# Optimization experiments

Hardware: AMD Instinct MI355X
Metric: run time of the kernel (lower is better)

The kernel has to match this reference:

```python
import jax, jax.numpy as jnp
import numpy as np

N_NODES = 50000
N_EDGES = 800000
IN_DIM = 64
OUT_DIM = 64
EDGE_DIM = 16
LN_EPS = 1e-5


def setup_inputs() -> dict:
    key = jax.random.key(0)
    ks = jax.random.split(key, 12)
    def lin(k, fan_in, fan_out):
        # torch nn.Linear default init: U(-1/sqrt(fan_in), 1/sqrt(fan_in))
        kw, kb = jax.random.split(k)
        bound = 1.0 / np.sqrt(fan_in)
        W = jax.random.uniform(kw, (fan_in, fan_out), jnp.float32, -bound, bound)
        b = jax.random.uniform(kb, (fan_out,), jnp.float32, -bound, bound)
        return W, b
    x = jax.random.normal(ks[0], (N_NODES, IN_DIM), jnp.float32)
    edge_index = jax.random.randint(ks[1], (2, N_EDGES), 0, N_NODES, jnp.int64 if jax.config.jax_enable_x64 else jnp.int32)
    edge_features = jax.random.normal(ks[2], (N_EDGES, EDGE_DIM), jnp.float32)
    W1, b1 = lin(ks[3], IN_DIM + EDGE_DIM, OUT_DIM)   # msg_mlp layer 1
    W2, b2 = lin(ks[4], OUT_DIM, OUT_DIM)             # msg_mlp layer 2
    W3, b3 = lin(ks[5], IN_DIM + OUT_DIM, OUT_DIM)    # update_mlp
    gamma = jnp.ones((OUT_DIM,), jnp.float32)
    beta = jnp.zeros((OUT_DIM,), jnp.float32)
    return {"x": x, "edge_index": edge_index, "edge_features": edge_features,
            "W1": W1, "b1": b1, "W2": W2, "b2": b2, "W3": W3, "b3": b3,
            "gamma": gamma, "beta": beta}


def reference(x, edge_index, edge_features, W1, b1, W2, b2, W3, b3, gamma, beta):
    num_nodes = x.shape[0]
    src, dst = edge_index[0], edge_index[1]
    # gather source node feats, concat with edge feats -> message MLP
    msg_in = jnp.concatenate([x[src], edge_features], axis=-1)           # [E, in+edge]
    h = jax.nn.relu(msg_in @ W1 + b1)
    messages = h @ W2 + b2                                               # [E, out]
    # scatter-add aggregate + mean by in-degree (count + 1e-8)
    agg = jax.ops.segment_sum(messages, dst, num_segments=num_nodes)     # [N, out]
    cnt = jax.ops.segment_sum(jnp.ones((messages.shape[0],), x.dtype), dst,
                              num_segments=num_nodes)[:, None]           # [N, 1]
    agg = agg / (cnt + 1e-8)
    # update MLP + residual (Identity since in_dim == out_dim) + LayerNorm
    updated = jax.nn.relu(jnp.concatenate([x, agg], axis=-1) @ W3 + b3)  # [N, out]
    y = updated + x
    mu = jnp.mean(y, axis=-1, keepdims=True)
    var = jnp.var(y, axis=-1, keepdims=True)
    return (y - mu) * jax.lax.rsqrt(var + LN_EPS) * gamma + beta
```

## Files before the change

kernel.cpp:

```cpp
#include <hip/hip_runtime.h>

typedef unsigned short u16;
typedef unsigned int u32;
typedef short short8 __attribute__((ext_vector_type(8)));
typedef short short4v __attribute__((ext_vector_type(4)));
typedef float floatx4 __attribute__((ext_vector_type(4)));

#define NE 800000
#define NNODES 50000
#define NBLK 196

#define LDS_FENCE() __asm__ volatile("s_waitcnt lgkmcnt(0)" ::: "memory")

__device__ __forceinline__ u16 f2bf(float f) {
    union { float f; unsigned int i; } v; v.f = f;
    return (u16)((v.i + 0x7fffu + ((v.i >> 16) & 1u)) >> 16);
}
__device__ __forceinline__ float bf2f(u16 u) {
    union { unsigned int i; float f; } v; v.i = ((unsigned int)u) << 16; return v.f;
}
__device__ __forceinline__ short8 pack8(const float4 a, const float4 b) {
    short8 o;
    o[0] = (short)f2bf(a.x); o[1] = (short)f2bf(a.y);
    o[2] = (short)f2bf(a.z); o[3] = (short)f2bf(a.w);
    o[4] = (short)f2bf(b.x); o[5] = (short)f2bf(b.y);
    o[6] = (short)f2bf(b.z); o[7] = (short)f2bf(b.w);
    return o;
}
__device__ __forceinline__ short8 ld8_bf(const float* __restrict__ p) {
    return pack8(*(const float4*)p, *(const float4*)(p + 4));
}

#define MFMA16(a, b, c) __builtin_amdgcn_mfma_f32_16x16x32_bf16(a, b, c, 0, 0, 0)

__global__ __launch_bounds__(256) void prep_kernel(
    const float* __restrict__ x, const int* __restrict__ ei,
    int* __restrict__ hist, u16* __restrict__ xbf)
{
    const int id = blockIdx.x * 256 + threadIdx.x;
    if (id < NE) atomicAdd(&hist[ei[NE + id]], 1);
    if (id < NNODES * 8) {
        *(short8*)&xbf[(size_t)id * 8] = ld8_bf(x + (size_t)id * 8);
    }
}

__global__ __launch_bounds__(256) void scan1_kernel(
    const int* __restrict__ hist, int* __restrict__ cursor, int* __restrict__ bsum)
{
    const int i = blockIdx.x * 256 + threadIdx.x;
    const int lane = threadIdx.x & 63;
    const int w = threadIdx.x >> 6;
    const int v = (i < NNODES) ? hist[i] : 0;
    int inc = v;
    #pragma unroll
    for (int o = 1; o < 64; o <<= 1) {
        const int tt = __shfl_up(inc, o);
        if (lane >= o) inc += tt;
    }
    __shared__ int ws[4];
    if (lane == 63) ws[w] = inc;
    __syncthreads();
    int add = 0;
    for (int j = 0; j < w; ++j) add += ws[j];
    const int excl = inc - v + add;
    if (i < NNODES) cursor[i] = excl;
    if (threadIdx.x == 255) bsum[blockIdx.x] = excl + v;
}

__global__ __launch_bounds__(256) void scan2_kernel(
    const int* __restrict__ bsum, int* __restrict__ bsumx)
{
    const int tid = threadIdx.x;
    const int lane = tid & 63;
    const int w = tid >> 6;
    const int v = (tid < NBLK) ? bsum[tid] : 0;
    int inc = v;
    #pragma unroll
    for (int o = 1; o < 64; o <<= 1) {
        const int tt = __shfl_up(inc, o);
        if (lane >= o) inc += tt;
    }
    __shared__ int ws[4];
    if (lane == 63) ws[w] = inc;
    __syncthreads();
    int add = 0;
    for (int j = 0; j < w; ++j) add += ws[j];
    bsumx[tid] = inc - v + add;
}

__global__ __launch_bounds__(256) void scatter_kernel(
    const int* __restrict__ ei, int* __restrict__ cursor,
    const int* __restrict__ bsumx, uint2* __restrict__ sde)
{
    const int e = blockIdx.x * 256 + threadIdx.x;
    if (e < NE) {
        const int dst = ei[NE + e];
        const int p = atomicAdd(&cursor[dst], 1) + bsumx[dst >> 8];
        uint2 v;
        v.x = (u32)e;
        v.y = ((u32)ei[e] << 16) | (u32)dst;
        sde[p] = v;
    }
}

__global__ __launch_bounds__(256) void edge_kernel(
    const u16* __restrict__ xbf, const float* __restrict__ ef,
    const float* __restrict__ w1, const float* __restrict__ b1,
    const float* __restrict__ w2, const float* __restrict__ b2,
    const uint2* __restrict__ sde, float* __restrict__ agg)
{
    constexpr int S1 = 104;
    constexpr int S2 = 72;
    __shared__ u16 A1[4][16 * S1];
    __shared__ u16 Hs[4][16 * S2];
    __shared__ int Ds[4][16];
    __shared__ u16 W2f[2][4][64 * 8];

    const int wid  = threadIdx.x >> 6;
    const int lane = threadIdx.x & 63;
    const int q    = lane >> 4;
    const int c    = lane & 15;
    const int r4   = lane >> 2;
    const int p4   = lane & 3;

    short8 w1f[3][4];
    #pragma unroll
    for (int kk = 0; kk < 3; ++kk)
        #pragma unroll
        for (int nn = 0; nn < 4; ++nn)
            #pragma unroll
            for (int j = 0; j < 8; ++j) {
                const int k = kk * 32 + q * 8 + j;
                w1f[kk][nn][j] = (k < 80) ? (short)f2bf(w1[k * 64 + nn * 16 + c]) : (short)0;
            }
    if (wid == 0) {
        #pragma unroll
        for (int kk = 0; kk < 2; ++kk)
            #pragma unroll
            for (int nn = 0; nn < 4; ++nn) {
                short8 f;
                #pragma unroll
                for (int j = 0; j < 8; ++j) {
                    const int k = kk * 32 + q * 8 + j;
                    f[j] = (short)f2bf(w2[k * 64 + nn * 16 + c]);
                }
                *(short8*)&W2f[kk][nn][lane * 8] = f;
            }
    }
    float b1v[4], b2v[4];
    #pragma unroll
    for (int nn = 0; nn < 4; ++nn) {
        b1v[nn] = b1[nn * 16 + c];
        b2v[nn] = b2[nn * 16 + c];
    }
    if (q == 1) {
        const short8 z8 = {0, 0, 0, 0, 0, 0, 0, 0};
        *(short8*)&A1[wid][c * S1 + 80] = z8;
        *(short8*)&A1[wid][c * S1 + 88] = z8;
    }
    __syncthreads();

    const floatx4 zero = {0.f, 0.f, 0.f, 0.f};
    const int ntile = NE / 16;
    const int stride = gridDim.x * 4;
    int t = blockIdx.x * 4 + wid;

    uint2 sdB; u32 eB;
    short8 xa, xb; float4 ev;
    int dcur;
    {
        const uint2 sdA = sde[t * 16 + c];
        const u32  eA  = sde[t * 16 + r4].x;
        dcur = (int)(sdA.y & 0xffffu);
        const int sA = (int)(sdA.y >> 16);
        int tb = t + stride; if (tb >= ntile) tb = ntile - 1;
        sdB = sde[tb * 16 + c];
        eB  = sde[tb * 16 + r4].x;
        const u16* xp = xbf + (size_t)sA * 64 + q * 16;
        xa = *(const short8*)xp;
        xb = *(const short8*)(xp + 8);
        ev = *(const float4*)(ef + (size_t)eA * 16 + p4 * 4);
    }

    for (; t < ntile; t += stride) {
        u16* arow = &A1[wid][c * S1 + q * 16];
        *(short8*)arow       = xa;
        *(short8*)(arow + 8) = xb;
        {
            short4v e4;
            e4[0] = (short)f2bf(ev.x); e4[1] = (short)f2bf(ev.y);
            e4[2] = (short)f2bf(ev.z); e4[3] = (short)f2bf(ev.w);
            *(short4v*)&A1[wid][r4 * S1 + 64 + p4 * 4] = e4;
        }
        if (q == 0) Ds[wid][c] = dcur;
        LDS_FENCE();

        short8 a1k[3];
        #pragma unroll
        for (int kk = 0; kk < 3; ++kk)
            a1k[kk] = *(const short8*)&A1[wid][c * S1 + kk * 32 + q * 8];

        const int dnext = (int)(sdB.y & 0xffffu);
        {
            const int sN = (int)(sdB.y >> 16);
            const u16* xp = xbf + (size_t)sN * 64 + q * 16;
            xa = *(const short8*)xp;
            xb = *(const short8*)(xp + 8);
            ev = *(const float4*)(ef + (size_t)eB * 16 + p4 * 4);
        }
        {
            int tb = t + 2 * stride; if (tb >= ntile) tb = ntile - 1;
            sdB = sde[tb * 16 + c];
            eB  = sde[tb * 16 + r4].x;
        }

        #pragma unroll
        for (int nn = 0; nn < 4; ++nn) {
            floatx4 acc = MFMA16(a1k[0], w1f[0][nn], zero);
            acc = MFMA16(a1k[1], w1f[1][nn], acc);
            acc = MFMA16(a1k[2], w1f[2][nn], acc);
            #pragma unroll
            for (int r = 0; r < 4; ++r) {
                const float h = fmaxf(acc[r] + b1v[nn], 0.f);
                Hs[wid][(q * 4 + r) * S2 + nn * 16 + c] = f2bf(h);
            }
        }
        LDS_FENCE();

        short8 a2k[2];
        #pragma unroll
        for (int kk = 0; kk < 2; ++kk)
            a2k[kk] = *(const short8*)&Hs[wid][c * S2 + kk * 32 + q * 8];

        #pragma unroll
        for (int nn = 0; nn < 4; ++nn) {
            const short8 wf0 = *(const short8*)&W2f[0][nn][lane * 8];
            const short8 wf1 = *(const short8*)&W2f[1][nn][lane * 8];
            floatx4 mg = MFMA16(a2k[0], wf0, zero);
            mg = MFMA16(a2k[1], wf1, mg);
            #pragma unroll
            for (int r = 0; r < 4; ++r)
                Hs[wid][(q * 4 + r) * S2 + nn * 16 + c] = f2bf(mg[r] + b2v[nn]);
        }
        LDS_FENCE();

        int dc = Ds[wid][0];
        float acc = bf2f(Hs[wid][lane]);
        #pragma unroll
        for (int row = 1; row < 16; ++row) {
            const int d = Ds[wid][row];
            const float v = bf2f(Hs[wid][row * S2 + lane]);
            if (d == dc) {
                acc += v;
            } else {
                atomicAdd(&agg[(size_t)dc * 64 + lane], acc);
                dc = d;
                acc = v;
            }
        }
        atomicAdd(&agg[(size_t)dc * 64 + lane], acc);

        dcur = dnext;
    }
}

__global__ __launch_bounds__(256) void node_kernel(
    const u16* __restrict__ xbf, const float* __restrict__ w3,
    const float* __restrict__ b3, const float* __restrict__ g,
    const float* __restrict__ bb, const float* __restrict__ agg,
    const int* __restrict__ hist, float* __restrict__ out)
{
    constexpr int S3 = 136;
    __shared__ u16 Cs[4][16 * S3];

    const int wid  = threadIdx.x >> 6;
    const int lane = threadIdx.x & 63;
    const int q    = lane >> 4;
    const int c    = lane & 15;

    short8 w3f[4][4];
    #pragma unroll
    for (int kk = 0; kk < 4; ++kk)
        #pragma unroll
        for (int nn = 0; nn < 4; ++nn)
            #pragma unroll
            for (int j = 0; j < 8; ++j) {
                const int k = kk * 32 + q * 8 + j;
                w3f[kk][nn][j] = (short)f2bf(w3[k * 64 + nn * 16 + c]);
            }
    float b3v[4], gv[4], bv[4];
    #pragma unroll
    for (int nn = 0; nn < 4; ++nn) {
        b3v[nn] = b3[nn * 16 + c];
        gv[nn]  = g[nn * 16 + c];
        bv[nn]  = bb[nn * 16 + c];
    }

    const floatx4 zero = {0.f, 0.f, 0.f, 0.f};
    const int ntile = NNODES / 16;

    for (int t = blockIdx.x * 4 + wid; t < ntile; t += gridDim.x * 4) {
        const int n0 = t * 16;
        const int node = n0 + c;
        u16* crow = &Cs[wid][c * S3];

        if (q < 2) {
            const u16* xp = xbf + (size_t)node * 64 + q * 32;
            *(short8*)&crow[q * 32]      = *(const short8*)xp;
            *(short8*)&crow[q * 32 + 8]  = *(const short8*)(xp + 8);
            *(short8*)&crow[q * 32 + 16] = *(const short8*)(xp + 16);
            *(short8*)&crow[q * 32 + 24] = *(const short8*)(xp + 24);
        } else {
            const int p = q - 2;
            const float inv = 1.0f / ((float)hist[node] + 1e-8f);
            const float* ap = agg + (size_t)node * 64 + p * 32;
            #pragma unroll
            for (int gi = 0; gi < 4; ++gi) {
                const float4 v0 = *(const float4*)(ap + gi * 8);
                const float4 v1 = *(const float4*)(ap + gi * 8 + 4);
                short8 o;
                o[0] = (short)f2bf(v0.x * inv);
                o[1] = (short)f2bf(v0.y * inv);
                o[2] = (short)f2bf(v0.z * inv);
                o[3] = (short)f2bf(v0.w * inv);
                o[4] = (short)f2bf(v1.x * inv);
                o[5] = (short)f2bf(v1.y * inv);
                o[6] = (short)f2bf(v1.z * inv);
                o[7] = (short)f2bf(v1.w * inv);
                *(short8*)&crow[64 + p * 32 + gi * 8] = o;
            }
        }
        LDS_FENCE();

        short8 af[4];
        #pragma unroll
        for (int kk = 0; kk < 4; ++kk)
            af[kk] = *(const short8*)&Cs[wid][c * S3 + kk * 32 + q * 8];

        float y[4][4];
        float s[4]  = {0.f, 0.f, 0.f, 0.f};
        float ss[4] = {0.f, 0.f, 0.f, 0.f};
        #pragma unroll
        for (int nn = 0; nn < 4; ++nn) {
            floatx4 acc = MFMA16(af[0], w3f[0][nn], zero);
            acc = MFMA16(af[1], w3f[1][nn], acc);
            acc = MFMA16(af[2], w3f[2][nn], acc);
            acc = MFMA16(af[3], w3f[3][nn], acc);
            #pragma unroll
            for (int r = 0; r < 4; ++r) {
                const float upd = fmaxf(acc[r] + b3v[nn], 0.f);
                const float xv = bf2f(Cs[wid][(q * 4 + r) * S3 + nn * 16 + c]);
                const float yy = upd + xv;
                y[r][nn] = yy;
                s[r] += yy;
                ss[r] += yy * yy;
            }
        }

        #pragma unroll
        for (int r = 0; r < 4; ++r) {
            float sr = s[r], sq = ss[r];
            #pragma unroll
            for (int off = 1; off < 16; off <<= 1) {
                sr += __shfl_xor(sr, off);
                sq += __shfl_xor(sq, off);
            }
            const float mu  = sr * (1.0f / 64.0f);
            const float var = sq * (1.0f / 64.0f) - mu * mu;
            const float rs  = rsqrtf(var + 1e-5f);
            float* op = out + (size_t)(n0 + q * 4 + r) * 64 + c;
            #pragma unroll
            for (int nn = 0; nn < 4; ++nn)
                op[nn * 16] = (y[r][nn] - mu) * rs * gv[nn] + bv[nn];
        }
    }
}

extern "C" void kernel_launch(void* const* d_in, const int* in_sizes, int n_in,
                              void* d_out, int out_size, void* d_ws, size_t ws_size,
                              hipStream_t stream) {
    const float* x   = (const float*)d_in[0];
    const int*   ei  = (const int*)d_in[1];
    const float* ef  = (const float*)d_in[2];
    const float* w1  = (const float*)d_in[3];
    const float* b1  = (const float*)d_in[4];
    const float* w2  = (const float*)d_in[5];
    const float* b2  = (const float*)d_in[6];
    const float* w3  = (const float*)d_in[7];
    const float* b3  = (const float*)d_in[8];
    const float* g   = (const float*)d_in[9];
    const float* bb  = (const float*)d_in[10];

    float* agg   = (float*)d_ws;
    int* hist    = (int*)d_ws + 3200000;
    int* cursor  = hist + NNODES;
    int* bsum    = cursor + NNODES;
    int* bsumx   = bsum + 256;
    u16* xbf     = (u16*)(bsumx + 256);
    uint2* sde   = (uint2*)((int*)d_ws + 4900512);

    hipMemsetAsync(d_ws, 0, (size_t)(3200000 + NNODES) * sizeof(float), stream);
    prep_kernel<<<3125, 256, 0, stream>>>(x, ei, hist, xbf);
    scan1_kernel<<<NBLK, 256, 0, stream>>>(hist, cursor, bsum);
    scan2_kernel<<<1, 256, 0, stream>>>(bsum, bsumx);
    scatter_kernel<<<3125, 256, 0, stream>>>(ei, cursor, bsumx, sde);
    edge_kernel<<<2048, 256, 0, stream>>>(xbf, ef, w1, b1, w2, b2, sde, agg);
    node_kernel<<<782, 256, 0, stream>>>(xbf, w3, b3, g, bb, agg, hist, (float*)d_out);
}
```

Before: 287.5 us.

## Fuse all stages into one persistent cooperative kernel with grid syncs

Replaces the memset and six separate launches with a single cooperative kernel. The phases are zeroing, histogram plus bf16 conversion, two scan steps, scatter, the edge MLP and the node MLP, separated by grid.sync(), with shared memory overlaid in a union. This removes per-launch overhead and the gaps between kernels. In exchange the grid is capped by occupancy (at most 1280 blocks), small phases such as the single-block scan leave most of the GPU idle at a grid barrier, and the edge phase now runs with fewer blocks than the previous 2048.

```diff
diff --git a/kernel.cpp b/kernel.cpp
--- a/kernel.cpp
+++ b/kernel.cpp
@@ -1,4 +1,7 @@
 #include <hip/hip_runtime.h>
+#include <hip/hip_cooperative_groups.h>
+
+namespace cg = cooperative_groups;
 
 typedef unsigned short u16;
 typedef unsigned int u32;
@@ -19,7 +22,9 @@
 __device__ __forceinline__ float bf2f(u16 u) {
     union { unsigned int i; float f; } v; v.i = ((unsigned int)u) << 16; return v.f;
 }
-__device__ __forceinline__ short8 pack8(const float4 a, const float4 b) {
+__device__ __forceinline__ short8 ld8_bf(const float* __restrict__ p) {
+    const float4 a = *(const float4*)p;
+    const float4 b = *(const float4*)(p + 4);
     short8 o;
     o[0] = (short)f2bf(a.x); o[1] = (short)f2bf(a.y);
     o[2] = (short)f2bf(a.z); o[3] = (short)f2bf(a.w);
@@ -27,73 +32,99 @@
     o[6] = (short)f2bf(b.z); o[7] = (short)f2bf(b.w);
     return o;
 }
-__device__ __forceinline__ short8 ld8_bf(const float* __restrict__ p) {
-    return pack8(*(const float4*)p, *(const float4*)(p + 4));
-}
 
 #define MFMA16(a, b, c) __builtin_amdgcn_mfma_f32_16x16x32_bf16(a, b, c, 0, 0, 0)
 
-__global__ __launch_bounds__(256) void prep_kernel(
+union SMem {
+    struct {
+        u16 A1[4][16 * 104];
+        u16 Hs[4][16 * 72];
+        u16 W2f[2][4][64 * 8];
+        int Ds[4][16];
+    } e;
+    struct {
+        u16 Cs[4][16 * 136];
+    } n;
+    struct {
+        int ws[4];
+    } s;
+};
+
+__global__ __launch_bounds__(256, 4) void fused_kernel(
     const float* __restrict__ x, const int* __restrict__ ei,
-    int* __restrict__ hist, u16* __restrict__ xbf)
+    const float* __restrict__ ef, const float* __restrict__ w1,
+    const float* __restrict__ b1, const float* __restrict__ w2,
+    const float* __restrict__ b2, const float* __restrict__ w3,
+    const float* __restrict__ b3, const float* __restrict__ g,
+    const float* __restrict__ bb, int* __restrict__ ws_base,
+    float* __restrict__ out)
 {
-    const int id = blockIdx.x * 256 + threadIdx.x;
-    if (id < NE) atomicAdd(&hist[ei[NE + id]], 1);
-    if (id < NNODES * 8) {
-        *(short8*)&xbf[(size_t)id * 8] = ld8_bf(x + (size_t)id * 8);
-    }
-}
-
-__global__ __launch_bounds__(256) void scan1_kernel(
-    const int* __restrict__ hist, int* __restrict__ cursor, int* __restrict__ bsum)
-{
-    const int i = blockIdx.x * 256 + threadIdx.x;
+    cg::grid_group grid = cg::this_grid();
+    __shared__ SMem sm;
+
+    float* agg   = (float*)ws_base;
+    int* hist    = ws_base + 3200000;
+    int* cursor  = hist + NNODES;
+    int* bsum    = cursor + NNODES;
+    int* bsumx   = bsum + 256;
+    u16* xbf     = (u16*)(bsumx + 256);
+    uint2* sde   = (uint2*)(ws_base + 4900512);
+
+    const int tid  = blockIdx.x * 256 + threadIdx.x;
+    const int nthr = gridDim.x * 256;
+    const int wid  = threadIdx.x >> 6;
     const int lane = threadIdx.x & 63;
-    const int w = threadIdx.x >> 6;
-    const int v = (i < NNODES) ? hist[i] : 0;
-    int inc = v;
-    #pragma unroll
-    for (int o = 1; o < 64; o <<= 1) {
-        const int tt = __shfl_up(inc, o);
-        if (lane >= o) inc += tt;
-    }
-    __shared__ int ws[4];
-    if (lane == 63) ws[w] = inc;
-    __syncthreads();
-    int add = 0;
-    for (int j = 0; j < w; ++j) add += ws[j];
-    const int excl = inc - v + add;
-    if (i < NNODES) cursor[i] = excl;
-    if (threadIdx.x == 255) bsum[blockIdx.x] = excl + v;
-}
-
-__global__ __launch_bounds__(256) void scan2_kernel(
-    const int* __restrict__ bsum, int* __restrict__ bsumx)
-{
-    const int tid = threadIdx.x;
-    const int lane = tid & 63;
-    const int w = tid >> 6;
-    const int v = (tid < NBLK) ? bsum[tid] : 0;
-    int inc = v;
-    #pragma unroll
-    for (int o = 1; o < 64; o <<= 1) {
-        const int tt = __shfl_up(inc, o);
-        if (lane >= o) inc += tt;
-    }
-    __shared__ int ws[4];
-    if (lane == 63) ws[w] = inc;
-    __syncthreads();
-    int add = 0;
-    for (int j = 0; j < w; ++j) add += ws[j];
-    bsumx[tid] = inc - v + add;
-}
-
-__global__ __launch_bounds__(256) void scatter_kernel(
-    const int* __restrict__ ei, int* __restrict__ cursor,
-    const int* __restrict__ bsumx, uint2* __restrict__ sde)
-{
-    const int e = blockIdx.x * 256 + threadIdx.x;
-    if (e < NE) {
+    const int q    = lane >> 4;
+    const int c    = lane & 15;
+
+    {
+        float4* zb = (float4*)ws_base;
+        const float4 z4 = {0.f, 0.f, 0.f, 0.f};
+        for (int i = tid; i < 825000; i += nthr) zb[i] = z4;
+    }
+    grid.sync();
+
+    for (int i = tid; i < NE; i += nthr) atomicAdd(&hist[ei[NE + i]], 1);
+    for (int i = tid; i < NNODES * 8; i += nthr)
+        *(short8*)&xbf[(size_t)i * 8] = ld8_bf(x + (size_t)i * 8);
+    grid.sync();
+
+    if (blockIdx.x < NBLK) {
+        const int i = blockIdx.x * 256 + threadIdx.x;
+        const int v = (i < NNODES) ? hist[i] : 0;
+        int inc = v;
+        #pragma unroll
+        for (int o = 1; o < 64; o <<= 1) {
+            const int tt = __shfl_up(inc, o);
+            if (lane >= o) inc += tt;
+        }
+        if (lane == 63) sm.s.ws[wid] = inc;
+        __syncthreads();
+        int add = 0;
+        for (int j = 0; j < wid; ++j) add += sm.s.ws[j];
+        const int excl = inc - v + add;
+        if (i < NNODES) cursor[i] = excl;
+        if (threadIdx.x == 255) bsum[blockIdx.x] = excl + v;
+    }
+    grid.sync();
+
+    if (blockIdx.x == 0) {
+        const int v = (threadIdx.x < NBLK) ? bsum[threadIdx.x] : 0;
+        int inc = v;
+        #pragma unroll
+        for (int o = 1; o < 64; o <<= 1) {
+            const int tt = __shfl_up(inc, o);
+            if (lane >= o) inc += tt;
+        }
+        if (lane == 63) sm.s.ws[wid] = inc;
+        __syncthreads();
+        int add = 0;
+        for (int j = 0; j < wid; ++j) add += sm.s.ws[j];
+        bsumx[threadIdx.x] = inc - v + add;
+    }
+    grid.sync();
+
+    for (int e = tid; e < NE; e += nthr) {
         const int dst = ei[NE + e];
         const int p = atomicAdd(&cursor[dst], 1) + bsumx[dst >> 8];
         uint2 v;
@@ -101,277 +132,254 @@
         v.y = ((u32)ei[e] << 16) | (u32)dst;
         sde[p] = v;
     }
-}
-
-__global__ __launch_bounds__(256) void edge_kernel(
-    const u16* __restrict__ xbf, const float* __restrict__ ef,
-    const float* __restrict__ w1, const float* __restrict__ b1,
-    const float* __restrict__ w2, const float* __restrict__ b2,
-    const uint2* __restrict__ sde, float* __restrict__ agg)
-{
-    constexpr int S1 = 104;
-    constexpr int S2 = 72;
-    __shared__ u16 A1[4][16 * S1];
-    __shared__ u16 Hs[4][16 * S2];
-    __shared__ int Ds[4][16];
-    __shared__ u16 W2f[2][4][64 * 8];
-
-    const int wid  = threadIdx.x >> 6;
-    const int lane = threadIdx.x & 63;
-    const int q    = lane >> 4;
-    const int c    = lane & 15;
-    const int r4   = lane >> 2;
-    const int p4   = lane & 3;
-
-    short8 w1f[3][4];
-    #pragma unroll
-    for (int kk = 0; kk < 3; ++kk)
-        #pragma unroll
-        for (int nn = 0; nn < 4; ++nn)
-            #pragma unroll
-            for (int j = 0; j < 8; ++j) {
-                const int k = kk * 32 + q * 8 + j;
-                w1f[kk][nn][j] = (k < 80) ? (short)f2bf(w1[k * 64 + nn * 16 + c]) : (short)0;
-            }
-    if (wid == 0) {
-        #pragma unroll
-        for (int kk = 0; kk < 2; ++kk)
-            #pragma unroll
-            for (int nn = 0; nn < 4; ++nn) {
-                short8 f;
+    grid.sync();
+
+    {
+        constexpr int S1 = 104;
+        constexpr int S2 = 72;
+        const int r4 = lane >> 2;
+        const int p4 = lane & 3;
+
+        short8 w1f[3][4];
+        #pragma unroll
+        for (int kk = 0; kk < 3; ++kk)
+            #pragma unroll
+            for (int nn = 0; nn < 4; ++nn)
                 #pragma unroll
                 for (int j = 0; j < 8; ++j) {
                     const int k = kk * 32 + q * 8 + j;
-                    f[j] = (short)f2bf(w2[k * 64 + nn * 16 + c]);
-                }
-                *(short8*)&W2f[kk][nn][lane * 8] = f;
-            }
-    }
-    float b1v[4], b2v[4];
-    #pragma unroll
-    for (int nn = 0; nn < 4; ++nn) {
-        b1v[nn] = b1[nn * 16 + c];
-        b2v[nn] = b2[nn * 16 + c];
-    }
-    if (q == 1) {
-        const short8 z8 = {0, 0, 0, 0, 0, 0, 0, 0};
-        *(short8*)&A1[wid][c * S1 + 80] = z8;
-        *(short8*)&A1[wid][c * S1 + 88] = z8;
-    }
-    __syncthreads();
-
-    const floatx4 zero = {0.f, 0.f, 0.f, 0.f};
-    const int ntile = NE / 16;
-    const int stride = gridDim.x * 4;
-    int t = blockIdx.x * 4 + wid;
-
-    uint2 sdB; u32 eB;
-    short8 xa, xb; float4 ev;
-    int dcur;
-    {
-        const uint2 sdA = sde[t * 16 + c];
-        const u32  eA  = sde[t * 16 + r4].x;
-        dcur = (int)(sdA.y & 0xffffu);
-        const int sA = (int)(sdA.y >> 16);
-        int tb = t + stride; if (tb >= ntile) tb = ntile - 1;
-        sdB = sde[tb * 16 + c];
-        eB  = sde[tb * 16 + r4].x;
-        const u16* xp = xbf + (size_t)sA * 64 + q * 16;
-        xa = *(const short8*)xp;
-        xb = *(const short8*)(xp + 8);
-        ev = *(const float4*)(ef + (size_t)eA * 16 + p4 * 4);
-    }
-
-    for (; t < ntile; t += stride) {
-        u16* arow = &A1[wid][c * S1 + q * 16];
-        *(short8*)arow       = xa;
-        *(short8*)(arow + 8) = xb;
+                    w1f[kk][nn][j] = (k < 80) ? (short)f2bf(w1[k * 64 + nn * 16 + c]) : (short)0;
+                }
+        if (wid == 0) {
+            #pragma unroll
+            for (int kk = 0; kk < 2; ++kk)
+                #pragma unroll
+                for (int nn = 0; nn < 4; ++nn) {
+                    short8 f;
+                    #pragma unroll
+                    for (int j = 0; j < 8; ++j) {
+                        const int k = kk * 32 + q * 8 + j;
+                        f[j] = (short)f2bf(w2[k * 64 + nn * 16 + c]);
+                    }
+                    *(short8*)&sm.e.W2f[kk][nn][lane * 8] = f;
+                }
+        }
+        float b1v[4], b2v[4];
+        #pragma unroll
+        for (int nn = 0; nn < 4; ++nn) {
+            b1v[nn] = b1[nn * 16 + c];
+            b2v[nn] = b2[nn * 16 + c];
+        }
+        __syncthreads();
+        if (q == 1) {
+            const short8 z8 = {0, 0, 0, 0, 0, 0, 0, 0};
+            *(short8*)&sm.e.A1[wid][c * S1 + 80] = z8;
+            *(short8*)&sm.e.A1[wid][c * S1 + 88] = z8;
+        }
+
+        const floatx4 zero = {0.f, 0.f, 0.f, 0.f};
+        const int ntile = NE / 16;
+        const int stride = gridDim.x * 4;
+        int t = blockIdx.x * 4 + wid;
+
+        uint2 sdB; u32 eB;
+        short8 xa, xb; float4 ev;
+        int dcur;
         {
-            short4v e4;
-            e4[0] = (short)f2bf(ev.x); e4[1] = (short)f2bf(ev.y);
-            e4[2] = (short)f2bf(ev.z); e4[3] = (short)f2bf(ev.w);
-            *(short4v*)&A1[wid][r4 * S1 + 64 + p4 * 4] = e4;
-        }
-        if (q == 0) Ds[wid][c] = dcur;
-        LDS_FENCE();
-
-        short8 a1k[3];
-        #pragma unroll
-        for (int kk = 0; kk < 3; ++kk)
-            a1k[kk] = *(const short8*)&A1[wid][c * S1 + kk * 32 + q * 8];
-
-        const int dnext = (int)(sdB.y & 0xffffu);
-        {
-            const int sN = (int)(sdB.y >> 16);
-            const u16* xp = xbf + (size_t)sN * 64 + q * 16;
+            const uint2 sdA = sde[t * 16 + c];
+            const u32  eA  = sde[t * 16 + r4].x;
+            dcur = (int)(sdA.y & 0xffffu);
+            const int sA = (int)(sdA.y >> 16);
+            int tb = t + stride; if (tb >= ntile) tb = ntile - 1;
+            sdB = sde[tb * 16 + c];
+            eB  = sde[tb * 16 + r4].x;
+            const u16* xp = xbf + (size_t)sA * 64 + q * 16;
             xa = *(const short8*)xp;
             xb = *(const short8*)(xp + 8);
-            ev = *(const float4*)(ef + (size_t)eB * 16 + p4 * 4);
-        }
-        {
-            int tb = t + 2 * stride; if (tb >= ntile) tb = ntile - 1;
-            sdB = sde[tb * 16 + c];
-            eB  = sde[tb * 16 + r4].x;
-        }
-
+            ev = *(const float4*)(ef + (size_t)eA * 16 + p4 * 4);
+        }
+
+        for (; t < ntile; t += stride) {
+            u16* arow = &sm.e.A1[wid][c * S1 + q * 16];
+            *(short8*)arow       = xa;
+            *(short8*)(arow + 8) = xb;
+            {
+                short4v e4;
+                e4[0] = (short)f2bf(ev.x); e4[1] = (short)f2bf(ev.y);
+                e4[2] = (short)f2bf(ev.z); e4[3] = (short)f2bf(ev.w);
+                *(short4v*)&sm.e.A1[wid][r4 * S1 + 64 + p4 * 4] = e4;
+            }
+            if (q == 0) sm.e.Ds[wid][c] = dcur;
+            LDS_FENCE();
+
+            short8 a1k[3];
+            #pragma unroll
+            for (int kk = 0; kk < 3; ++kk)
+                a1k[kk] = *(const short8*)&sm.e.A1[wid][c * S1 + kk * 32 + q * 8];
+
+            const int dnext = (int)(sdB.y & 0xffffu);
+            {
+                const int sN = (int)(sdB.y >> 16);
+                const u16* xp = xbf + (size_t)sN * 64 + q * 16;
+                xa = *(const short8*)xp;
+                xb = *(const short8*)(xp + 8);
+                ev = *(const float4*)(ef + (size_t)eB * 16 + p4 * 4);
+            }
+            {
+                int tb = t + 2 * stride; if (tb >= ntile) tb = ntile - 1;
+                sdB = sde[tb * 16 + c];
+                eB  = sde[tb * 16 + r4].x;
+            }
+
+            #pragma unroll
+            for (int nn = 0; nn < 4; ++nn) {
+                floatx4 acc = MFMA16(a1k[0], w1f[0][nn], zero);
+                acc = MFMA16(a1k[1], w1f[1][nn], acc);
+                acc = MFMA16(a1k[2], w1f[2][nn], acc);
+                #pragma unroll
+                for (int r = 0; r < 4; ++r) {
+                    const float h = fmaxf(acc[r] + b1v[nn], 0.f);
+                    sm.e.Hs[wid][(q * 4 + r) * S2 + nn * 16 + c] = f2bf(h);
+                }
+            }
+            LDS_FENCE();
+
+            short8 a2k[2];
+            #pragma unroll
+            for (int kk = 0; kk < 2; ++kk)
+                a2k[kk] = *(const short8*)&sm.e.Hs[wid][c * S2 + kk * 32 + q * 8];
+
+            #pragma unroll
+            for (int nn = 0; nn < 4; ++nn) {
+                const short8 wf0 = *(const short8*)&sm.e.W2f[0][nn][lane * 8];
+                const short8 wf1 = *(const short8*)&sm.e.W2f[1][nn][lane * 8];
+                floatx4 mg = MFMA16(a2k[0], wf0, zero);
+                mg = MFMA16(a2k[1], wf1, mg);
+                #pragma unroll
+                for (int r = 0; r < 4; ++r)
+                    sm.e.Hs[wid][(q * 4 + r) * S2 + nn * 16 + c] = f2bf(mg[r] + b2v[nn]);
+            }
+            LDS_FENCE();
+
+            int dc = sm.e.Ds[wid][0];
+            float acc = bf2f(sm.e.Hs[wid][lane]);
+            #pragma unroll
+            for (int row = 1; row < 16; ++row) {
+                const int d = sm.e.Ds[wid][row];
+                const float v = bf2f(sm.e.Hs[wid][row * S2 + lane]);
+                if (d == dc) {
+                    acc += v;
+                } else {
+                    atomicAdd(&agg[(size_t)dc * 64 + lane], acc);
+                    dc = d;
+                    acc = v;
+                }
+            }
+            atomicAdd(&agg[(size_t)dc * 64 + lane], acc);
+
+            dcur = dnext;
+        }
+    }
+    grid.sync();
+
+    {
+        constexpr int S3 = 136;
+
+        short8 w3f[4][4];
+        #pragma unroll
+        for (int kk = 0; kk < 4; ++kk)
+            #pragma unroll
+            for (int nn = 0; nn < 4; ++nn)
+                #pragma unroll
+                for (int j = 0; j < 8; ++j) {
+                    const int k = kk * 32 + q * 8 + j;
+                    w3f[kk][nn][j] = (short)f2bf(w3[k * 64 + nn * 16 + c]);
+                }
+        float b3v[4], gv[4], bv[4];
         #pragma unroll
         for (int nn = 0; nn < 4; ++nn) {
-            floatx4 acc = MFMA16(a1k[0], w1f[0][nn], zero);
-            acc = MFMA16(a1k[1], w1f[1][nn], acc);
-            acc = MFMA16(a1k[2], w1f[2][nn], acc);
+            b3v[nn] = b3[nn * 16 + c];
+            gv[nn]  = g[nn * 16 + c];
+            bv[nn]  = bb[nn * 16 + c];
+        }
+
+        const floatx4 zero = {0.f, 0.f, 0.f, 0.f};
+        const int ntile = NNODES / 16;
+
+        for (int t = blockIdx.x * 4 + wid; t < ntile; t += gridDim.x * 4) {
+            const int n0 = t * 16;
+            const int node = n0 + c;
+            u16* crow = &sm.n.Cs[wid][c * S3];
+
+            if (q < 2) {
+                const u16* xp = xbf + (size_t)node * 64 + q * 32;
+                *(short8*)&crow[q * 32]      = *(const short8*)xp;
+                *(short8*)&crow[q * 32 + 8]  = *(const short8*)(xp + 8);
+                *(short8*)&crow[q * 32 + 16] = *(const short8*)(xp + 16);
+                *(short8*)&crow[q * 32 + 24] = *(const short8*)(xp + 24);
+            } else {
+                const int p = q - 2;
+                const float inv = 1.0f / ((float)hist[node] + 1e-8f);
+                const float* ap = agg + (size_t)node * 64 + p * 32;
+                #pragma unroll
+                for (int gi = 0; gi < 4; ++gi) {
+                    const float4 v0 = *(const float4*)(ap + gi * 8);
+                    const float4 v1 = *(const float4*)(ap + gi * 8 + 4);
+                    short8 o;
+                    o[0] = (short)f2bf(v0.x * inv);
+                    o[1] = (short)f2bf(v0.y * inv);
+                    o[2] = (short)f2bf(v0.z * inv);
+                    o[3] = (short)f2bf(v0.w * inv);
+                    o[4] = (short)f2bf(v1.x * inv);
+                    o[5] = (short)f2bf(v1.y * inv);
+                    o[6] = (short)f2bf(v1.z * inv);
+                    o[7] = (short)f2bf(v1.w * inv);
+                    *(short8*)&crow[64 + p * 32 + gi * 8] = o;
+                }
+            }
+            LDS_FENCE();
+
+            short8 af[4];
+            #pragma unroll
+            for (int kk = 0; kk < 4; ++kk)
+                af[kk] = *(const short8*)&sm.n.Cs[wid][c * S3 + kk * 32 + q * 8];
+
+            float y[4][4];
+            float s[4]  = {0.f, 0.f, 0.f, 0.f};
+            float ss[4] = {0.f, 0.f, 0.f, 0.f};
+            #pragma unroll
+            for (int nn = 0; nn < 4; ++nn) {
+                floatx4 acc = MFMA16(af[0], w3f[0][nn], zero);
+                acc = MFMA16(af[1], w3f[1][nn], acc);
+                acc = MFMA16(af[2], w3f[2][nn], acc);
+                acc = MFMA16(af[3], w3f[3][nn], acc);
+                #pragma unroll
+                for (int r = 0; r < 4; ++r) {
+                    const float upd = fmaxf(acc[r] + b3v[nn], 0.f);
+                    const float xv = bf2f(sm.n.Cs[wid][(q * 4 + r) * S3 + nn * 16 + c]);
+                    const float yy = upd + xv;
+                    y[r][nn] = yy;
+                    s[r] += yy;
+                    ss[r] += yy * yy;
+                }
+            }
+
             #pragma unroll
             for (int r = 0; r < 4; ++r) {
-                const float h = fmaxf(acc[r] + b1v[nn], 0.f);
-                Hs[wid][(q * 4 + r) * S2 + nn * 16 + c] = f2bf(h);
-            }
-        }
-        LDS_FENCE();
-
-        short8 a2k[2];
-        #pragma unroll
-        for (int kk = 0; kk < 2; ++kk)
-            a2k[kk] = *(const short8*)&Hs[wid][c * S2 + kk * 32 + q * 8];
-
-        #pragma unroll
-        for (int nn = 0; nn < 4; ++nn) {
-            const short8 wf0 = *(const short8*)&W2f[0][nn][lane * 8];
-            const short8 wf1 = *(const short8*)&W2f[1][nn][lane * 8];
-            floatx4 mg = MFMA16(a2k[0], wf0, zero);
-            mg = MFMA16(a2k[1], wf1, mg);
-            #pragma unroll
-            for (int r = 0; r < 4; ++r)
-                Hs[wid][(q * 4 + r) * S2 + nn * 16 + c] = f2bf(mg[r] + b2v[nn]);
-        }
-        LDS_FENCE();
-
-        int dc = Ds[wid][0];
-        float acc = bf2f(Hs[wid][lane]);
-        #pragma unroll
-        for (int row = 1; row < 16; ++row) {
-            const int d = Ds[wid][row];
-            const float v = bf2f(Hs[wid][row * S2 + lane]);
-            if (d == dc) {
-                acc += v;
-            } else {
-                atomicAdd(&agg[(size_t)dc * 64 + lane], acc);
-                dc = d;
-                acc = v;
-            }
-        }
-        atomicAdd(&agg[(size_t)dc * 64 + lane], acc);
-
-        dcur = dnext;
-    }
-}
-
-__global__ __launch_bounds__(256) void node_kernel(
-    const u16* __restrict__ xbf, const float* __restrict__ w3,
-    const float* __restrict__ b3, const float* __restrict__ g,
-    const float* __restrict__ bb, const float* __restrict__ agg,
-    const int* __restrict__ hist, float* __restrict__ out)
-{
-    constexpr int S3 = 136;
-    __shared__ u16 Cs[4][16 * S3];
-
-    const int wid  = threadIdx.x >> 6;
-    const int lane = threadIdx.x & 63;
-    const int q    = lane >> 4;
-    const int c    = lane & 15;
-
-    short8 w3f[4][4];
-    #pragma unroll
-    for (int kk = 0; kk < 4; ++kk)
-        #pragma unroll
-        for (int nn = 0; nn < 4; ++nn)
-            #pragma unroll
-            for (int j = 0; j < 8; ++j) {
-                const int k = kk * 32 + q * 8 + j;
-                w3f[kk][nn][j] = (short)f2bf(w3[k * 64 + nn * 16 + c]);
-            }
-    float b3v[4], gv[4], bv[4];
-    #pragma unroll
-    for (int nn = 0; nn < 4; ++nn) {
-        b3v[nn] = b3[nn * 16 + c];
-        gv[nn]  = g[nn * 16 + c];
-        bv[nn]  = bb[nn * 16 + c];
-    }
-
-    const floatx4 zero = {0.f, 0.f, 0.f, 0.f};
-    const int ntile = NNODES / 16;
-
-    for (int t = blockIdx.x * 4 + wid; t < ntile; t += gridDim.x * 4) {
-        const int n0 = t * 16;
-        const int node = n0 + c;
-        u16* crow = &Cs[wid][c * S3];
-
-        if (q < 2) {
-            const u16* xp = xbf + (size_t)node * 64 + q * 32;
-            *(short8*)&crow[q * 32]      = *(const short8*)xp;
-            *(short8*)&crow[q * 32 + 8]  = *(const short8*)(xp + 8);
-            *(short8*)&crow[q * 32 + 16] = *(const short8*)(xp + 16);
-            *(short8*)&crow[q * 32 + 24] = *(const short8*)(xp + 24);
-        } else {
-            const int p = q - 2;
-            const float inv = 1.0f / ((float)hist[node] + 1e-8f);
-            const float* ap = agg + (size_t)node * 64 + p * 32;
-            #pragma unroll
-            for (int gi = 0; gi < 4; ++gi) {
-                const float4 v0 = *(const float4*)(ap + gi * 8);
-                const float4 v1 = *(const float4*)(ap + gi * 8 + 4);
-                short8 o;
-                o[0] = (short)f2bf(v0.x * inv);
-                o[1] = (short)f2bf(v0.y * inv);
-                o[2] = (short)f2bf(v0.z * inv);
-                o[3] = (short)f2bf(v0.w * inv);
-                o[4] = (short)f2bf(v1.x * inv);
-                o[5] = (short)f2bf(v1.y * inv);
-                o[6] = (short)f2bf(v1.z * inv);
-                o[7] = (short)f2bf(v1.w * inv);
-                *(short8*)&crow[64 + p * 32 + gi * 8] = o;
-            }
-        }
-        LDS_FENCE();
-
-        short8 af[4];
-        #pragma unroll
-        for (int kk = 0; kk < 4; ++kk)
-            af[kk] = *(const short8*)&Cs[wid][c * S3 + kk * 32 + q * 8];
-
-        float y[4][4];
-        float s[4]  = {0.f, 0.f, 0.f, 0.f};
-        float ss[4] = {0.f, 0.f, 0.f, 0.f};
-        #pragma unroll
-        for (int nn = 0; nn < 4; ++nn) {
-            floatx4 acc = MFMA16(af[0], w3f[0][nn], zero);
-            acc = MFMA16(af[1], w3f[1][nn], acc);
-            acc = MFMA16(af[2], w3f[2][nn], acc);
-            acc = MFMA16(af[3], w3f[3][nn], acc);
-            #pragma unroll
-            for (int r = 0; r < 4; ++r) {
-                const float upd = fmaxf(acc[r] + b3v[nn], 0.f);
-                const float xv = bf2f(Cs[wid][(q * 4 + r) * S3 + nn * 16 + c]);
-                const float yy = upd + xv;
-                y[r][nn] = yy;
-                s[r] += yy;
-                ss[r] += yy * yy;
-            }
-        }
-
-        #pragma unroll
-        for (int r = 0; r < 4; ++r) {
-            float sr = s[r], sq = ss[r];
-            #pragma unroll
-            for (int off = 1; off < 16; off <<= 1) {
-                sr += __shfl_xor(sr, off);
-                sq += __shfl_xor(sq, off);
-            }
-            const float mu  = sr * (1.0f / 64.0f);
-            const float var = sq * (1.0f / 64.0f) - mu * mu;
-            const float rs  = rsqrtf(var + 1e-5f);
-            float* op = out + (size_t)(n0 + q * 4 + r) * 64 + c;
-            #pragma unroll
-            for (int nn = 0; nn < 4; ++nn)
-                op[nn * 16] = (y[r][nn] - mu) * rs * gv[nn] + bv[nn];
+                float sr = s[r], sq = ss[r];
+                #pragma unroll
+                for (int off = 1; off < 16; off <<= 1) {
+                    sr += __shfl_xor(sr, off);
+                    sq += __shfl_xor(sq, off);
+                }
+                const float mu  = sr * (1.0f / 64.0f);
+                const float var = sq * (1.0f / 64.0f) - mu * mu;
+                const float rs  = rsqrtf(var + 1e-5f);
+                float* op = out + (size_t)(n0 + q * 4 + r) * 64 + c;
+                #pragma unroll
+                for (int nn = 0; nn < 4; ++nn)
+                    op[nn * 16] = (y[r][nn] - mu) * rs * gv[nn] + bv[nn];
+            }
         }
     }
 }
@@ -390,20 +398,19 @@
     const float* b3  = (const float*)d_in[8];
     const float* g   = (const float*)d_in[9];
     const float* bb  = (const float*)d_in[10];
-
-    float* agg   = (float*)d_ws;
-    int* hist    = (int*)d_ws + 3200000;
-    int* cursor  = hist + NNODES;
-    int* bsum    = cursor + NNODES;
-    int* bsumx   = bsum + 256;
-    u16* xbf     = (u16*)(bsumx + 256);
-    uint2* sde   = (uint2*)((int*)d_ws + 4900512);
-
-    hipMemsetAsync(d_ws, 0, (size_t)(3200000 + NNODES) * sizeof(float), stream);
-    prep_kernel<<<3125, 256, 0, stream>>>(x, ei, hist, xbf);
-    scan1_kernel<<<NBLK, 256, 0, stream>>>(hist, cursor, bsum);
-    scan2_kernel<<<1, 256, 0, stream>>>(bsum, bsumx);
-    scatter_kernel<<<3125, 256, 0, stream>>>(ei, cursor, bsumx, sde);
-    edge_kernel<<<2048, 256, 0, stream>>>(xbf, ef, w1, b1, w2, b2, sde, agg);
-    node_kernel<<<782, 256, 0, stream>>>(xbf, w3, b3, g, bb, agg, hist, (float*)d_out);
+    int* ws  = (int*)d_ws;
+    float* out = (float*)d_out;
+
+    int maxb = 4;
+    hipOccupancyMaxActiveBlocksPerMultiprocessor(&maxb, fused_kernel, 256, 0);
+    if (maxb < 1) maxb = 1;
+    int grid = maxb * 256;
+    if (grid > 1280) grid = 1280;
+    if (grid < 256) grid = 256;
+
+    void* args[] = { (void*)&x, (void*)&ei, (void*)&ef, (void*)&w1, (void*)&b1,
+                     (void*)&w2, (void*)&b2, (void*)&w3, (void*)&b3, (void*)&g,
+                     (void*)&bb, (void*)&ws, (void*)&out };
+    hipLaunchCooperativeKernel((void*)fused_kernel, dim3(grid), dim3(256),
+                               args, 0, stream);
 }
```

Measured after the change: 673.5 us. 134% more time.

## Fuse memset, histogram, scan and scatter into one cooperative kernel

Applied to the files above, without the earlier changes.

The memset plus the four preprocessing kernels (histogram/bf16 conversion, two scan passes, CSR scatter) become a single cooperative kernel that uses grid-wide syncs between phases. Zeroing of hist and agg moves into the kernel, and the second-level scan is recomputed redundantly in every block in shared memory. This removes several launch gaps and the memset call. In exchange it adds grid.sync barriers, runs a smaller persistent grid with grid-stride loops, and calls an occupancy query on the host at every launch.

```diff
diff --git a/kernel.cpp b/kernel.cpp
--- a/kernel.cpp
+++ b/kernel.cpp
@@ -1,4 +1,7 @@
 #include <hip/hip_runtime.h>
+#include <hip/hip_cooperative_groups.h>
+
+namespace cg = cooperative_groups;
 
 typedef unsigned short u16;
 typedef unsigned int u32;
@@ -19,7 +22,9 @@
 __device__ __forceinline__ float bf2f(u16 u) {
     union { unsigned int i; float f; } v; v.i = ((unsigned int)u) << 16; return v.f;
 }
-__device__ __forceinline__ short8 pack8(const float4 a, const float4 b) {
+__device__ __forceinline__ short8 ld8_bf(const float* __restrict__ p) {
+    const float4 a = *(const float4*)p;
+    const float4 b = *(const float4*)(p + 4);
     short8 o;
     o[0] = (short)f2bf(a.x); o[1] = (short)f2bf(a.y);
     o[2] = (short)f2bf(a.z); o[3] = (short)f2bf(a.w);
@@ -27,79 +32,88 @@
     o[6] = (short)f2bf(b.z); o[7] = (short)f2bf(b.w);
     return o;
 }
-__device__ __forceinline__ short8 ld8_bf(const float* __restrict__ p) {
-    return pack8(*(const float4*)p, *(const float4*)(p + 4));
-}
 
 #define MFMA16(a, b, c) __builtin_amdgcn_mfma_f32_16x16x32_bf16(a, b, c, 0, 0, 0)
 
-__global__ __launch_bounds__(256) void prep_kernel(
+__global__ __launch_bounds__(256) void aux_kernel(
     const float* __restrict__ x, const int* __restrict__ ei,
-    int* __restrict__ hist, u16* __restrict__ xbf)
+    int* __restrict__ ws_base)
 {
-    const int id = blockIdx.x * 256 + threadIdx.x;
-    if (id < NE) atomicAdd(&hist[ei[NE + id]], 1);
-    if (id < NNODES * 8) {
-        *(short8*)&xbf[(size_t)id * 8] = ld8_bf(x + (size_t)id * 8);
-    }
-}
-
-__global__ __launch_bounds__(256) void scan1_kernel(
-    const int* __restrict__ hist, int* __restrict__ cursor, int* __restrict__ bsum)
-{
-    const int i = blockIdx.x * 256 + threadIdx.x;
+    cg::grid_group grid = cg::this_grid();
+    __shared__ int ws[4];
+    __shared__ int bsx[256];
+
+    float* agg   = (float*)ws_base;
+    int* hist    = ws_base + 3200000;
+    int* cursor  = hist + NNODES;
+    int* bsum    = cursor + NNODES;
+    u16* xbf     = (u16*)(bsum + 512);
+    uint2* sde   = (uint2*)(ws_base + 4900512);
+
+    const int tid  = blockIdx.x * 256 + threadIdx.x;
+    const int nthr = gridDim.x * 256;
+    const int wid  = threadIdx.x >> 6;
     const int lane = threadIdx.x & 63;
-    const int w = threadIdx.x >> 6;
-    const int v = (i < NNODES) ? hist[i] : 0;
-    int inc = v;
-    #pragma unroll
-    for (int o = 1; o < 64; o <<= 1) {
-        const int tt = __shfl_up(inc, o);
-        if (lane >= o) inc += tt;
-    }
-    __shared__ int ws[4];
-    if (lane == 63) ws[w] = inc;
-    __syncthreads();
-    int add = 0;
-    for (int j = 0; j < w; ++j) add += ws[j];
-    const int excl = inc - v + add;
-    if (i < NNODES) cursor[i] = excl;
-    if (threadIdx.x == 255) bsum[blockIdx.x] = excl + v;
-}
-
-__global__ __launch_bounds__(256) void scan2_kernel(
-    const int* __restrict__ bsum, int* __restrict__ bsumx)
-{
-    const int tid = threadIdx.x;
-    const int lane = tid & 63;
-    const int w = tid >> 6;
-    const int v = (tid < NBLK) ? bsum[tid] : 0;
-    int inc = v;
-    #pragma unroll
-    for (int o = 1; o < 64; o <<= 1) {
-        const int tt = __shfl_up(inc, o);
-        if (lane >= o) inc += tt;
-    }
-    __shared__ int ws[4];
-    if (lane == 63) ws[w] = inc;
-    __syncthreads();
-    int add = 0;
-    for (int j = 0; j < w; ++j) add += ws[j];
-    bsumx[tid] = inc - v + add;
-}
-
-__global__ __launch_bounds__(256) void scatter_kernel(
-    const int* __restrict__ ei, int* __restrict__ cursor,
-    const int* __restrict__ bsumx, uint2* __restrict__ sde)
-{
-    const int e = blockIdx.x * 256 + threadIdx.x;
-    if (e < NE) {
-        const int dst = ei[NE + e];
-        const int p = atomicAdd(&cursor[dst], 1) + bsumx[dst >> 8];
-        uint2 v;
-        v.x = (u32)e;
-        v.y = ((u32)ei[e] << 16) | (u32)dst;
-        sde[p] = v;
+
+    {
+        int4* hb = (int4*)hist;
+        const int4 z4 = {0, 0, 0, 0};
+        for (int i = tid; i < NNODES / 4; i += nthr) hb[i] = z4;
+    }
+    grid.sync();
+
+    for (int i = tid; i < NE; i += nthr) atomicAdd(&hist[ei[NE + i]], 1);
+    for (int i = tid; i < NNODES * 8; i += nthr)
+        *(short8*)&xbf[(size_t)i * 8] = ld8_bf(x + (size_t)i * 8);
+    {
+        float4* ab = (float4*)agg;
+        const float4 z4 = {0.f, 0.f, 0.f, 0.f};
+        for (int i = tid; i < NNODES * 16; i += nthr) ab[i] = z4;
+    }
+    grid.sync();
+
+    if (blockIdx.x < NBLK) {
+        const int i = blockIdx.x * 256 + threadIdx.x;
+        const int v = (i < NNODES) ? hist[i] : 0;
+        int inc = v;
+        #pragma unroll
+        for (int o = 1; o < 64; o <<= 1) {
+            const int tt = __shfl_up(inc, o);
+            if (lane >= o) inc += tt;
+        }
+        if (lane == 63) ws[wid] = inc;
+        __syncthreads();
+        int add = 0;
+        for (int j = 0; j < wid; ++j) add += ws[j];
+        const int excl = inc - v + add;
+        if (i < NNODES) cursor[i] = excl;
+        if (threadIdx.x == 255) bsum[blockIdx.x] = excl + v;
+    }
+    grid.sync();
+
+    {
+        const int v = (threadIdx.x < NBLK) ? bsum[threadIdx.x] : 0;
+        int inc = v;
+        #pragma unroll
+        for (int o = 1; o < 64; o <<= 1) {
+            const int tt = __shfl_up(inc, o);
+            if (lane >= o) inc += tt;
+        }
+        if (lane == 63) ws[wid] = inc;
+        __syncthreads();
+        int add = 0;
+        for (int j = 0; j < wid; ++j) add += ws[j];
+        bsx[threadIdx.x] = inc - v + add;
+        __syncthreads();
+
+        for (int e = tid; e < NE; e += nthr) {
+            const int dst = ei[NE + e];
+            const int p = atomicAdd(&cursor[dst], 1) + bsx[dst >> 8];
+            uint2 v2;
+            v2.x = (u32)e;
+            v2.y = ((u32)ei[e] << 16) | (u32)dst;
+            sde[p] = v2;
+        }
     }
 }
 
@@ -390,20 +404,24 @@
     const float* b3  = (const float*)d_in[8];
     const float* g   = (const float*)d_in[9];
     const float* bb  = (const float*)d_in[10];
-
-    float* agg   = (float*)d_ws;
-    int* hist    = (int*)d_ws + 3200000;
-    int* cursor  = hist + NNODES;
-    int* bsum    = cursor + NNODES;
-    int* bsumx   = bsum + 256;
-    u16* xbf     = (u16*)(bsumx + 256);
-    uint2* sde   = (uint2*)((int*)d_ws + 4900512);
-
-    hipMemsetAsync(d_ws, 0, (size_t)(3200000 + NNODES) * sizeof(float), stream);
-    prep_kernel<<<3125, 256, 0, stream>>>(x, ei, hist, xbf);
-    scan1_kernel<<<NBLK, 256, 0, stream>>>(hist, cursor, bsum);
-    scan2_kernel<<<1, 256, 0, stream>>>(bsum, bsumx);
-    scatter_kernel<<<3125, 256, 0, stream>>>(ei, cursor, bsumx, sde);
+    int* ws = (int*)d_ws;
+
+    float* agg = (float*)d_ws;
+    int* hist  = ws + 3200000;
+    u16* xbf   = (u16*)(ws + 3300512);
+    uint2* sde = (uint2*)(ws + 4900512);
+
+    int maxb = 8;
+    hipOccupancyMaxActiveBlocksPerMultiprocessor(&maxb, aux_kernel, 256, 0);
+    if (maxb < 1) maxb = 1;
+    int agrid = maxb * 256;
+    if (agrid > 512) agrid = 512;
+    if (agrid < NBLK) agrid = NBLK;
+
+    void* args[] = { (void*)&x, (void*)&ei, (void*)&ws };
+    hipLaunchCooperativeKernel((void*)aux_kernel, dim3(agrid), dim3(256),
+                               args, 0, stream);
     edge_kernel<<<2048, 256, 0, stream>>>(xbf, ef, w1, b1, w2, b2, sde, agg);
-    node_kernel<<<782, 256, 0, stream>>>(xbf, w3, b3, g, bb, agg, hist, (float*)d_out);
-}
+    node_kernel<<<782, 256, 0, stream>>>(xbf, w3, b3, g, bb, agg, hist,
+                                         (float*)d_out);
+}
```

After: 473.3 us. 1.65x slower.
